# Optimization experiments

Measured on AMD Instinct MI355X. Metric: run time of the kernel, lower is better.

Reference implementation:

```python
import jax, jax.numpy as jnp
import numpy as np


def xnorm(x, g):
    # x * gamma / ||x||_2 along last dim (no eps, matching torch.norm)
    n = jnp.sqrt(jnp.sum(x * x, axis=-1, keepdims=True))
    return x * g / n


def setup_inputs() -> dict:
    key = jax.random.key(0)
    ks = jax.random.split(key, 6)
    B, N, D = 8, 8192, 512
    H, DK, DV = 8, 64, 64
    std = 0.001
    return {
        "queries": jax.random.normal(ks[0], (B, N, D), dtype=jnp.float32),
        # weights stored [in, out] (transposed vs torch Linear)
        "Wq": jax.random.normal(ks[1], (D, H * DK), dtype=jnp.float32) * std,
        "bq": jnp.zeros((H * DK,), dtype=jnp.float32),
        "Wk": jax.random.normal(ks[2], (D, H * DK), dtype=jnp.float32) * std,
        "bk": jnp.zeros((H * DK,), dtype=jnp.float32),
        "Wv": jax.random.normal(ks[3], (D, H * DV), dtype=jnp.float32) * std,
        "bv": jnp.zeros((H * DV,), dtype=jnp.float32),
        "Wo": jax.random.normal(ks[4], (H * DV, D), dtype=jnp.float32) * std,
        "bo": jnp.zeros((D,), dtype=jnp.float32),
        "gamma": jax.random.normal(ks[5], (1, H, 1, 1), dtype=jnp.float32),
    }


def reference(queries, Wq, bq, Wk, bk, Wv, bv, Wo, bo, gamma):
    B, N, D = queries.shape
    H, DK = 8, 64
    DV = 64
    q = (queries @ Wq + bq).reshape(B, N, H, DK)  # bnhd
    k = (queries @ Wk + bk).reshape(B, N, H, DK)
    v = (queries @ Wv + bv).reshape(B, N, H, DV)
    # kv = k^T @ v per (batch, head): [B,H,DK,DV]
    kv = jnp.einsum("bnhk,bnhv->bhkv", k, v)
    kv_n = xnorm(kv, gamma)                       # norm over DV axis
    q_n = xnorm(q.transpose(0, 2, 1, 3), gamma)   # bhnd, norm over DK axis
    out = jnp.einsum("bhnk,bhkv->bnhv", q_n, kv_n).reshape(B, N, H * DV)
    return out @ Wo + bo
```

## Files before the change

### kernel.cpp

```cpp
#include <hip/hip_runtime.h>

typedef __attribute__((ext_vector_type(8))) short s8v;
typedef __attribute__((ext_vector_type(4))) short s4v;
typedef __attribute__((ext_vector_type(4))) float f4v;

__device__ __forceinline__ unsigned short f2bf(float f) {
  unsigned int u = __float_as_uint(f);
  u += 0x7FFFu + ((u >> 16) & 1u);
  return (unsigned short)(u >> 16);
}
__device__ __forceinline__ float bf2f(unsigned short s) {
  return __uint_as_float(((unsigned int)s) << 16);
}

__device__ __forceinline__ void gld16(const void* g, void* l) {
  __builtin_amdgcn_global_load_lds(
      (const __attribute__((address_space(1))) unsigned int*)g,
      (__attribute__((address_space(3))) unsigned int*)l, 16, 0, 0);
}

#define TILE_SYNC() asm volatile("s_waitcnt vmcnt(0) lgkmcnt(0)\n\ts_barrier" ::: "memory")

__global__ __launch_bounds__(256)
void convert_x_kernel(const float* __restrict__ X, unsigned short* __restrict__ Xbf)
{
  size_t base = ((size_t)blockIdx.x * 256 + threadIdx.x) * 8;
  float4 a = *(const float4*)&X[base];
  float4 b = *(const float4*)&X[base + 4];
  s8v p = (s8v){ (short)f2bf(a.x), (short)f2bf(a.y), (short)f2bf(a.z), (short)f2bf(a.w),
                 (short)f2bf(b.x), (short)f2bf(b.y), (short)f2bf(b.z), (short)f2bf(b.w) };
  *(s8v*)&Xbf[base] = p;
}

__global__ __launch_bounds__(256)
void transpose_w_kernel(const float* __restrict__ Wq, const float* __restrict__ Wk,
                        const float* __restrict__ Wv, unsigned short* __restrict__ Wt)
{
  __shared__ float T[64][68];
  const int kt = blockIdx.x, nt = blockIdx.y;
  const float* W = (nt < 8) ? Wq : (nt < 16 ? Wk : Wv);
  const int n0 = (nt & 7) * 64, k0 = kt * 64;
  const int t = threadIdx.x;
  #pragma unroll
  for (int it = 0; it < 4; ++it) {
    int idx = it * 256 + t;
    int k = idx >> 4, n4 = (idx & 15) << 2;
    *(float4*)&T[k][n4] = *(const float4*)&W[(size_t)(k0 + k) * 512 + n0 + n4];
  }
  __syncthreads();
  #pragma unroll
  for (int it = 0; it < 2; ++it) {
    int idx = it * 256 + t;
    int n = idx >> 3, k8 = (idx & 7) << 3;
    s8v p;
    #pragma unroll
    for (int j = 0; j < 8; ++j) p[j] = (short)f2bf(T[k8 + j][n]);
    *(s8v*)&Wt[((size_t)nt * 64 + n) * 512 + k0 + k8] = p;
  }
}

__global__ __launch_bounds__(256, 2)
void gemm_qkv_kernel(const unsigned short* __restrict__ Xbf,
                     const unsigned short* __restrict__ Wt,
                     const float* __restrict__ bq, const float* __restrict__ bk,
                     const float* __restrict__ bv,
                     const float* __restrict__ gamma,
                     unsigned short* __restrict__ qkv)
{
  __shared__ short As[2][8192];
  __shared__ short Bs[2][8192];
  const int t = threadIdx.x;
  const int o = blockIdx.x;
  const int swz = (o & 7) * 768 + (o >> 3);
  const int nb = swz % 12, rb = swz / 12;
  const int wave = t >> 6, lane = t & 63;
  const int wm = wave & 1, wn = wave >> 1;
  const int quad = lane >> 4, l16 = lane & 15;
  const int row0 = rb * 128;
  const int ncol0 = nb * 128;

  const unsigned short* ap[4];
  const unsigned short* bp[4];
  int ldst[4];
  #pragma unroll
  for (int i = 0; i < 4; ++i) {
    int s = i * 256 + t;
    int m = s >> 3;
    int kb = (s & 7) ^ (m & 7);
    ap[i] = Xbf + (size_t)(row0 + m) * 512 + kb * 8;
    bp[i] = Wt + (size_t)(ncol0 + m) * 512 + kb * 8;
    ldst[i] = s * 8;
  }

  f4v acc[4][4];
  #pragma unroll
  for (int i = 0; i < 4; ++i)
    #pragma unroll
    for (int j = 0; j < 4; ++j) acc[i][j] = (f4v){0.f, 0.f, 0.f, 0.f};

  #pragma unroll
  for (int i = 0; i < 4; ++i) {
    gld16(ap[i], &As[0][ldst[i]]);
    gld16(bp[i], &Bs[0][ldst[i]]);
  }
  TILE_SYNC();

  for (int kt = 0; kt < 8; ++kt) {
    const int cur = kt & 1;
    if (kt < 7) {
      const int koff = (kt + 1) * 64;
      #pragma unroll
      for (int i = 0; i < 4; ++i) {
        gld16(ap[i] + koff, &As[cur ^ 1][ldst[i]]);
        gld16(bp[i] + koff, &Bs[cur ^ 1][ldst[i]]);
      }
    }
    #pragma unroll
    for (int ks = 0; ks < 2; ++ks) {
      s8v a[4], b[4];
      #pragma unroll
      for (int mi = 0; mi < 4; ++mi) {
        int r = wm * 64 + mi * 16 + l16;
        int slot = r * 8 + ((ks * 4 + quad) ^ (r & 7));
        a[mi] = *(const s8v*)&As[cur][slot * 8];
      }
      #pragma unroll
      for (int nj = 0; nj < 4; ++nj) {
        int r = wn * 64 + nj * 16 + l16;
        int slot = r * 8 + ((ks * 4 + quad) ^ (r & 7));
        b[nj] = *(const s8v*)&Bs[cur][slot * 8];
      }
      #pragma unroll
      for (int mi = 0; mi < 4; ++mi)
        #pragma unroll
        for (int nj = 0; nj < 4; ++nj)
          acc[mi][nj] = __builtin_amdgcn_mfma_f32_16x16x32_bf16(a[mi], b[nj], acc[mi][nj], 0, 0, 0);
    }
    TILE_SYNC();
  }

  #pragma unroll
  for (int nj = 0; nj < 4; ++nj) {
    int colg = ncol0 + wn * 64 + nj * 16 + l16;
    float bias;
    if (colg < 512) bias = bq[colg];
    else if (colg < 1024) bias = bk[colg - 512];
    else bias = bv[colg - 1024];
    #pragma unroll
    for (int mi = 0; mi < 4; ++mi) {
      acc[mi][nj][0] += bias; acc[mi][nj][1] += bias;
      acc[mi][nj][2] += bias; acc[mi][nj][3] += bias;
    }
  }

  if (nb < 4) {
    float g = gamma[nb * 2 + wn];
    #pragma unroll
    for (int mi = 0; mi < 4; ++mi)
      #pragma unroll
      for (int rr = 0; rr < 4; ++rr) {
        float ss = acc[mi][0][rr] * acc[mi][0][rr] + acc[mi][1][rr] * acc[mi][1][rr]
                 + acc[mi][2][rr] * acc[mi][2][rr] + acc[mi][3][rr] * acc[mi][3][rr];
        ss += __shfl_xor(ss, 1);
        ss += __shfl_xor(ss, 2);
        ss += __shfl_xor(ss, 4);
        ss += __shfl_xor(ss, 8);
        float scale = g * rsqrtf(ss);
        acc[mi][0][rr] *= scale; acc[mi][1][rr] *= scale;
        acc[mi][2][rr] *= scale; acc[mi][3][rr] *= scale;
      }
  }

  const int colbase = ncol0 + wn * 64;
  #pragma unroll
  for (int mi = 0; mi < 4; ++mi)
    #pragma unroll
    for (int nj = 0; nj < 4; ++nj)
      #pragma unroll
      for (int rr = 0; rr < 4; ++rr) {
        int row = row0 + wm * 64 + mi * 16 + quad * 4 + rr;
        int col = colbase + nj * 16 + l16;
        qkv[(size_t)row * 1536 + col] = f2bf(acc[mi][nj][rr]);
      }
}

__global__ __launch_bounds__(256)
void kv_accum_kernel(const unsigned short* __restrict__ qkv, float* __restrict__ kvpart)
{
  __shared__ float ksf[16][64];
  __shared__ float vsf[16][64];
  const int t = threadIdx.x;
  const int bh = blockIdx.x, chunk = blockIdx.y;
  const int b = bh >> 3, h = bh & 7;
  const int base_row = b * 8192 + chunk * 512;
  const int lane = t & 63, wave = t >> 6;
  const int dk0 = (lane & 7) * 8, dv0 = (lane >> 3) * 8;
  const int half = t >> 7, tt = t & 127;
  const int sr = tt >> 3, u = tt & 7;
  const int col = (half ? 1024 : 512) + h * 64 + u * 8;
  const unsigned short* src = qkv + (size_t)(base_row + sr) * 1536 + col;
  float* dstlds = half ? &vsf[sr][u * 8] : &ksf[sr][u * 8];
  float acc[8][8] = {};

  for (int it = 0; it < 32; ++it) {
    __syncthreads();
    union { int4 v; unsigned short s[8]; } raw;
    raw.v = *(const int4*)(src + (size_t)it * 16 * 1536);
    float4 lo = { bf2f(raw.s[0]), bf2f(raw.s[1]), bf2f(raw.s[2]), bf2f(raw.s[3]) };
    float4 hi = { bf2f(raw.s[4]), bf2f(raw.s[5]), bf2f(raw.s[6]), bf2f(raw.s[7]) };
    *(float4*)dstlds = lo;
    *(float4*)(dstlds + 4) = hi;
    __syncthreads();
    #pragma unroll
    for (int rr = 0; rr < 4; ++rr) {
      int r = rr * 4 + wave;
      float4 ka = *(const float4*)&ksf[r][dk0];
      float4 kb = *(const float4*)&ksf[r][dk0 + 4];
      float4 va = *(const float4*)&vsf[r][dv0];
      float4 vb = *(const float4*)&vsf[r][dv0 + 4];
      float kf[8] = { ka.x, ka.y, ka.z, ka.w, kb.x, kb.y, kb.z, kb.w };
      float vf[8] = { va.x, va.y, va.z, va.w, vb.x, vb.y, vb.z, vb.w };
      #pragma unroll
      for (int i = 0; i < 8; ++i)
        #pragma unroll
        for (int j = 0; j < 8; ++j)
          acc[i][j] = fmaf(kf[i], vf[j], acc[i][j]);
    }
  }
  float* dst = kvpart + ((size_t)(chunk * 4 + wave) * 64 + bh) * 4096;
  #pragma unroll
  for (int i = 0; i < 8; ++i) {
    *(float4*)&dst[(dk0 + i) * 64 + dv0]     = (float4){ acc[i][0], acc[i][1], acc[i][2], acc[i][3] };
    *(float4*)&dst[(dk0 + i) * 64 + dv0 + 4] = (float4){ acc[i][4], acc[i][5], acc[i][6], acc[i][7] };
  }
}

__global__ __launch_bounds__(256)
void kv_reduce_kernel(const float* __restrict__ kvpart, float* __restrict__ kvbuf)
{
  const int bh = blockIdx.x, seg = blockIdx.y, t = threadIdx.x;
  #pragma unroll
  for (int e = 0; e < 2; ++e) {
    int i = seg * 512 + e * 256 + t;
    float s = 0.f;
    for (int c = 0; c < 64; ++c) s += kvpart[((size_t)c * 64 + bh) * 4096 + i];
    kvbuf[(size_t)bh * 4096 + i] = s;
  }
}

__global__ __launch_bounds__(256)
void build_w2t_kernel(const float* __restrict__ kvbuf, const float* __restrict__ Wo,
                      const float* __restrict__ gamma, unsigned short* __restrict__ W2t)
{
  __shared__ float WoS[512][16];
  const int b = blockIdx.x, dt = blockIdx.y;
  const int d0 = dt * 16;
  const int t = threadIdx.x;
  for (int i = 0; i < 32; ++i) {
    int flat = i * 256 + t;
    int rr_ = flat >> 4, c = flat & 15;
    WoS[rr_][c] = Wo[(size_t)rr_ * 512 + d0 + c];
  }
  __syncthreads();
  for (int rr = 0; rr < 2; ++rr) {
    int r = rr * 256 + t;
    int h = r >> 6, k = r & 63;
    const float* krow = kvbuf + ((size_t)b * 8 + h) * 4096 + (size_t)k * 64;
    float ss = 0.f;
    #pragma unroll
    for (int v = 0; v < 64; v += 4) {
      float4 x = *(const float4*)&krow[v];
      ss += x.x * x.x + x.y * x.y + x.z * x.z + x.w * x.w;
    }
    float scale = gamma[h] * rsqrtf(ss);
    f4v accv[4];
    #pragma unroll
    for (int j = 0; j < 4; ++j) accv[j] = (f4v){0.f, 0.f, 0.f, 0.f};
    for (int v = 0; v < 64; ++v) {
      float m = krow[v] * scale;
      const float* w = &WoS[h * 64 + v][0];
      #pragma unroll
      for (int j4 = 0; j4 < 4; ++j4) {
        float4 ww = *(const float4*)&w[j4 * 4];
        accv[j4][0] = fmaf(m, ww.x, accv[j4][0]);
        accv[j4][1] = fmaf(m, ww.y, accv[j4][1]);
        accv[j4][2] = fmaf(m, ww.z, accv[j4][2]);
        accv[j4][3] = fmaf(m, ww.w, accv[j4][3]);
      }
    }
    #pragma unroll
    for (int j = 0; j < 16; ++j)
      W2t[((size_t)b * 512 + d0 + j) * 512 + r] = f2bf(accv[j >> 2][j & 3]);
  }
}

__global__ __launch_bounds__(256, 2)
void gemm_out_kernel(const unsigned short* __restrict__ qkv,
                     const unsigned short* __restrict__ W2t,
                     const float* __restrict__ bo,
                     float* __restrict__ out)
{
  __shared__ short As[2][8192];
  __shared__ short Bs[2][8192];
  const int t = threadIdx.x;
  const int o = blockIdx.x;
  const int swz = (o & 7) * 256 + (o >> 3);
  const int nb = swz & 3, rb = swz >> 2;
  const int wave = t >> 6, lane = t & 63;
  const int wm = wave & 1, wn = wave >> 1;
  const int quad = lane >> 4, l16 = lane & 15;
  const int row0 = rb * 128;
  const int ncol0 = nb * 128;
  const unsigned short* Wb = W2t + (size_t)(rb >> 6) * 262144;

  const unsigned short* ap[4];
  const unsigned short* bp[4];
  int ldst[4];
  #pragma unroll
  for (int i = 0; i < 4; ++i) {
    int s = i * 256 + t;
    int m = s >> 3;
    int kb = (s & 7) ^ (m & 7);
    ap[i] = qkv + (size_t)(row0 + m) * 1536 + kb * 8;
    bp[i] = Wb + (size_t)(ncol0 + m) * 512 + kb * 8;
    ldst[i] = s * 8;
  }

  f4v acc[4][4];
  #pragma unroll
  for (int i = 0; i < 4; ++i)
    #pragma unroll
    for (int j = 0; j < 4; ++j) acc[i][j] = (f4v){0.f, 0.f, 0.f, 0.f};

  #pragma unroll
  for (int i = 0; i < 4; ++i) {
    gld16(ap[i], &As[0][ldst[i]]);
    gld16(bp[i], &Bs[0][ldst[i]]);
  }
  TILE_SYNC();

  for (int kt = 0; kt < 8; ++kt) {
    const int cur = kt & 1;
    if (kt < 7) {
      const int koff = (kt + 1) * 64;
      #pragma unroll
      for (int i = 0; i < 4; ++i) {
        gld16(ap[i] + koff, &As[cur ^ 1][ldst[i]]);
        gld16(bp[i] + koff, &Bs[cur ^ 1][ldst[i]]);
      }
    }
    #pragma unroll
    for (int ks = 0; ks < 2; ++ks) {
      s8v a[4], b[4];
      #pragma unroll
      for (int mi = 0; mi < 4; ++mi) {
        int r = wm * 64 + mi * 16 + l16;
        int slot = r * 8 + ((ks * 4 + quad) ^ (r & 7));
        a[mi] = *(const s8v*)&As[cur][slot * 8];
      }
      #pragma unroll
      for (int nj = 0; nj < 4; ++nj) {
        int r = wn * 64 + nj * 16 + l16;
        int slot = r * 8 + ((ks * 4 + quad) ^ (r & 7));
        b[nj] = *(const s8v*)&Bs[cur][slot * 8];
      }
      #pragma unroll
      for (int mi = 0; mi < 4; ++mi)
        #pragma unroll
        for (int nj = 0; nj < 4; ++nj)
          acc[mi][nj] = __builtin_amdgcn_mfma_f32_16x16x32_bf16(a[mi], b[nj], acc[mi][nj], 0, 0, 0);
    }
    TILE_SYNC();
  }

  const int colbase = ncol0 + wn * 64;
  #pragma unroll
  for (int nj = 0; nj < 4; ++nj) {
    float bias = bo[colbase + nj * 16 + l16];
    #pragma unroll
    for (int mi = 0; mi < 4; ++mi)
      #pragma unroll
      for (int rr = 0; rr < 4; ++rr) {
        int row = row0 + wm * 64 + mi * 16 + quad * 4 + rr;
        int col = colbase + nj * 16 + l16;
        out[(size_t)row * 512 + col] = acc[mi][nj][rr] + bias;
      }
  }
}

extern "C" void kernel_launch(void* const* d_in, const int* in_sizes, int n_in,
                              void* d_out, int out_size, void* d_ws, size_t ws_size,
                              hipStream_t stream)
{
  (void)in_sizes; (void)n_in; (void)out_size; (void)ws_size;
  const float* X     = (const float*)d_in[0];
  const float* Wq    = (const float*)d_in[1];
  const float* bq    = (const float*)d_in[2];
  const float* Wk    = (const float*)d_in[3];
  const float* bk    = (const float*)d_in[4];
  const float* Wv    = (const float*)d_in[5];
  const float* bv    = (const float*)d_in[6];
  const float* Wo    = (const float*)d_in[7];
  const float* bo    = (const float*)d_in[8];
  const float* gamma = (const float*)d_in[9];

  char* ws = (char*)d_ws;
  unsigned short* qkv = (unsigned short*)ws;
  unsigned short* Xbf = (unsigned short*)(ws + 201326592);
  float* kvpart = (float*)(ws + 201326592);
  unsigned short* Wt  = (unsigned short*)(ws + 201326592 + 67108864);
  float* kvbuf        = (float*)(ws + 201326592 + 67108864 + 1572864);
  unsigned short* W2t = (unsigned short*)(ws + 201326592 + 67108864 + 1572864 + 1048576);

  dim3 blk(256);
  convert_x_kernel<<<16384, blk, 0, stream>>>(X, Xbf);
  transpose_w_kernel<<<dim3(8, 24), blk, 0, stream>>>(Wq, Wk, Wv, Wt);
  gemm_qkv_kernel<<<6144, blk, 0, stream>>>(Xbf, Wt, bq, bk, bv, gamma, qkv);
  kv_accum_kernel<<<dim3(64, 16), blk, 0, stream>>>(qkv, kvpart);
  kv_reduce_kernel<<<dim3(64, 8), blk, 0, stream>>>(kvpart, kvbuf);
  build_w2t_kernel<<<dim3(8, 32), blk, 0, stream>>>(kvbuf, Wo, gamma, W2t);
  gemm_out_kernel<<<2048, blk, 0, stream>>>(qkv, W2t, bo, (float*)d_out);
}
```

Baseline: 551.9 us.

## Enlarge GEMM tiles to 256x256 with 8 waves and interleaved prefetch

Both bf16 GEMMs move from 128x128 tiles with 4 waves to 256x256 tiles with 8 waves (512 threads), so each wave computes a 128x64 output block. This raises operand reuse per LDS byte and cuts the block count by four. The K-loop is split into four MFMA phases with the next-tile global-to-LDS loads spread across them, barriers between phases, and s_setprio raised around the MFMA bursts. The cost is higher register pressure (8x4 accumulators), 128KB of LDS per block, which limits occupancy, and fewer blocks for load balancing.

```diff
diff --git a/kernel.cpp b/kernel.cpp
--- a/kernel.cpp
+++ b/kernel.cpp
@@ -59,7 +59,7 @@
   }
 }
 
-__global__ __launch_bounds__(256, 2)
+__global__ __launch_bounds__(512, 2)
 void gemm_qkv_kernel(const unsigned short* __restrict__ Xbf,
                      const unsigned short* __restrict__ Wt,
                      const float* __restrict__ bq, const float* __restrict__ bk,
@@ -67,34 +67,32 @@
                      const float* __restrict__ gamma,
                      unsigned short* __restrict__ qkv)
 {
-  __shared__ short As[2][8192];
-  __shared__ short Bs[2][8192];
+  __shared__ short As[2][16384];
+  __shared__ short Bs[2][16384];
   const int t = threadIdx.x;
   const int o = blockIdx.x;
-  const int swz = (o & 7) * 768 + (o >> 3);
-  const int nb = swz % 12, rb = swz / 12;
+  const int swz = (o & 7) * 192 + (o >> 3);
+  const int nb = swz % 6, rb = swz / 6;
   const int wave = t >> 6, lane = t & 63;
   const int wm = wave & 1, wn = wave >> 1;
   const int quad = lane >> 4, l16 = lane & 15;
-  const int row0 = rb * 128;
-  const int ncol0 = nb * 128;
+  const int row0 = rb * 256, ncol0 = nb * 256;
 
   const unsigned short* ap[4];
   const unsigned short* bp[4];
   int ldst[4];
   #pragma unroll
   for (int i = 0; i < 4; ++i) {
-    int s = i * 256 + t;
-    int m = s >> 3;
-    int kb = (s & 7) ^ (m & 7);
+    int s = i * 512 + t;
+    int m = s >> 3, kb = (s & 7) ^ (m & 7);
     ap[i] = Xbf + (size_t)(row0 + m) * 512 + kb * 8;
     bp[i] = Wt + (size_t)(ncol0 + m) * 512 + kb * 8;
     ldst[i] = s * 8;
   }
 
-  f4v acc[4][4];
-  #pragma unroll
-  for (int i = 0; i < 4; ++i)
+  f4v acc[8][4];
+  #pragma unroll
+  for (int i = 0; i < 8; ++i)
     #pragma unroll
     for (int j = 0; j < 4; ++j) acc[i][j] = (f4v){0.f, 0.f, 0.f, 0.f};
 
@@ -107,35 +105,89 @@
 
   for (int kt = 0; kt < 8; ++kt) {
     const int cur = kt & 1;
-    if (kt < 7) {
-      const int koff = (kt + 1) * 64;
-      #pragma unroll
-      for (int i = 0; i < 4; ++i) {
-        gld16(ap[i] + koff, &As[cur ^ 1][ldst[i]]);
-        gld16(bp[i] + koff, &Bs[cur ^ 1][ldst[i]]);
-      }
-    }
-    #pragma unroll
-    for (int ks = 0; ks < 2; ++ks) {
-      s8v a[4], b[4];
-      #pragma unroll
-      for (int mi = 0; mi < 4; ++mi) {
-        int r = wm * 64 + mi * 16 + l16;
-        int slot = r * 8 + ((ks * 4 + quad) ^ (r & 7));
-        a[mi] = *(const s8v*)&As[cur][slot * 8];
-      }
-      #pragma unroll
-      for (int nj = 0; nj < 4; ++nj) {
+    const short* Ac = As[cur];
+    const short* Bc = Bs[cur];
+    short* An = (short*)As[cur ^ 1];
+    short* Bn = (short*)Bs[cur ^ 1];
+    const int koff = (kt + 1) * 64;
+    const bool pf = kt < 7;
+    s8v afr[4][2], bfr[4][2];
+
+    if (pf) {
+      gld16(ap[0] + koff, &An[ldst[0]]);
+      gld16(ap[1] + koff, &An[ldst[1]]);
+      gld16(bp[0] + koff, &Bn[ldst[0]]);
+      gld16(bp[1] + koff, &Bn[ldst[1]]);
+    }
+    #pragma unroll
+    for (int nj = 0; nj < 4; ++nj)
+      #pragma unroll
+      for (int ks = 0; ks < 2; ++ks) {
         int r = wn * 64 + nj * 16 + l16;
-        int slot = r * 8 + ((ks * 4 + quad) ^ (r & 7));
-        b[nj] = *(const s8v*)&Bs[cur][slot * 8];
-      }
-      #pragma unroll
-      for (int mi = 0; mi < 4; ++mi)
-        #pragma unroll
-        for (int nj = 0; nj < 4; ++nj)
-          acc[mi][nj] = __builtin_amdgcn_mfma_f32_16x16x32_bf16(a[mi], b[nj], acc[mi][nj], 0, 0, 0);
-    }
+        bfr[nj][ks] = *(const s8v*)&Bc[(r * 8 + ((ks * 4 + quad) ^ (r & 7))) * 8];
+      }
+    #pragma unroll
+    for (int mi = 0; mi < 4; ++mi)
+      #pragma unroll
+      for (int ks = 0; ks < 2; ++ks) {
+        int r = wm * 128 + mi * 16 + l16;
+        afr[mi][ks] = *(const s8v*)&Ac[(r * 8 + ((ks * 4 + quad) ^ (r & 7))) * 8];
+      }
+    __builtin_amdgcn_s_setprio(1);
+    #pragma unroll
+    for (int mi = 0; mi < 4; ++mi)
+      #pragma unroll
+      for (int nj = 0; nj < 2; ++nj)
+        #pragma unroll
+        for (int ks = 0; ks < 2; ++ks)
+          acc[mi][nj] = __builtin_amdgcn_mfma_f32_16x16x32_bf16(afr[mi][ks], bfr[nj][ks], acc[mi][nj], 0, 0, 0);
+    __builtin_amdgcn_s_setprio(0);
+    __builtin_amdgcn_s_barrier();
+
+    if (pf) {
+      gld16(ap[2] + koff, &An[ldst[2]]);
+      gld16(ap[3] + koff, &An[ldst[3]]);
+      gld16(bp[2] + koff, &Bn[ldst[2]]);
+      gld16(bp[3] + koff, &Bn[ldst[3]]);
+    }
+    __builtin_amdgcn_s_setprio(1);
+    #pragma unroll
+    for (int mi = 0; mi < 4; ++mi)
+      #pragma unroll
+      for (int nj = 2; nj < 4; ++nj)
+        #pragma unroll
+        for (int ks = 0; ks < 2; ++ks)
+          acc[mi][nj] = __builtin_amdgcn_mfma_f32_16x16x32_bf16(afr[mi][ks], bfr[nj][ks], acc[mi][nj], 0, 0, 0);
+    __builtin_amdgcn_s_setprio(0);
+    __builtin_amdgcn_s_barrier();
+
+    #pragma unroll
+    for (int mi = 0; mi < 4; ++mi)
+      #pragma unroll
+      for (int ks = 0; ks < 2; ++ks) {
+        int r = wm * 128 + (4 + mi) * 16 + l16;
+        afr[mi][ks] = *(const s8v*)&Ac[(r * 8 + ((ks * 4 + quad) ^ (r & 7))) * 8];
+      }
+    __builtin_amdgcn_s_setprio(1);
+    #pragma unroll
+    for (int mi = 0; mi < 4; ++mi)
+      #pragma unroll
+      for (int nj = 0; nj < 2; ++nj)
+        #pragma unroll
+        for (int ks = 0; ks < 2; ++ks)
+          acc[4 + mi][nj] = __builtin_amdgcn_mfma_f32_16x16x32_bf16(afr[mi][ks], bfr[nj][ks], acc[4 + mi][nj], 0, 0, 0);
+    __builtin_amdgcn_s_setprio(0);
+    __builtin_amdgcn_s_barrier();
+
+    __builtin_amdgcn_s_setprio(1);
+    #pragma unroll
+    for (int mi = 0; mi < 4; ++mi)
+      #pragma unroll
+      for (int nj = 2; nj < 4; ++nj)
+        #pragma unroll
+        for (int ks = 0; ks < 2; ++ks)
+          acc[4 + mi][nj] = __builtin_amdgcn_mfma_f32_16x16x32_bf16(afr[mi][ks], bfr[nj][ks], acc[4 + mi][nj], 0, 0, 0);
+    __builtin_amdgcn_s_setprio(0);
     TILE_SYNC();
   }
 
@@ -147,16 +199,16 @@
     else if (colg < 1024) bias = bk[colg - 512];
     else bias = bv[colg - 1024];
     #pragma unroll
-    for (int mi = 0; mi < 4; ++mi) {
+    for (int mi = 0; mi < 8; ++mi) {
       acc[mi][nj][0] += bias; acc[mi][nj][1] += bias;
       acc[mi][nj][2] += bias; acc[mi][nj][3] += bias;
     }
   }
 
-  if (nb < 4) {
-    float g = gamma[nb * 2 + wn];
-    #pragma unroll
-    for (int mi = 0; mi < 4; ++mi)
+  if (nb < 2) {
+    float g = gamma[nb * 4 + wn];
+    #pragma unroll
+    for (int mi = 0; mi < 8; ++mi)
       #pragma unroll
       for (int rr = 0; rr < 4; ++rr) {
         float ss = acc[mi][0][rr] * acc[mi][0][rr] + acc[mi][1][rr] * acc[mi][1][rr]
@@ -173,12 +225,12 @@
 
   const int colbase = ncol0 + wn * 64;
   #pragma unroll
-  for (int mi = 0; mi < 4; ++mi)
+  for (int mi = 0; mi < 8; ++mi)
     #pragma unroll
     for (int nj = 0; nj < 4; ++nj)
       #pragma unroll
       for (int rr = 0; rr < 4; ++rr) {
-        int row = row0 + wm * 64 + mi * 16 + quad * 4 + rr;
+        int row = row0 + wm * 128 + mi * 16 + quad * 4 + rr;
         int col = colbase + nj * 16 + l16;
         qkv[(size_t)row * 1536 + col] = f2bf(acc[mi][nj][rr]);
       }
@@ -294,41 +346,39 @@
   }
 }
 
-__global__ __launch_bounds__(256, 2)
+__global__ __launch_bounds__(512, 2)
 void gemm_out_kernel(const unsigned short* __restrict__ qkv,
                      const unsigned short* __restrict__ W2t,
                      const float* __restrict__ bo,
                      float* __restrict__ out)
 {
-  __shared__ short As[2][8192];
-  __shared__ short Bs[2][8192];
+  __shared__ short As[2][16384];
+  __shared__ short Bs[2][16384];
   const int t = threadIdx.x;
   const int o = blockIdx.x;
-  const int swz = (o & 7) * 256 + (o >> 3);
-  const int nb = swz & 3, rb = swz >> 2;
+  const int swz = (o & 7) * 64 + (o >> 3);
+  const int nb = swz & 1, rb = swz >> 1;
   const int wave = t >> 6, lane = t & 63;
   const int wm = wave & 1, wn = wave >> 1;
   const int quad = lane >> 4, l16 = lane & 15;
-  const int row0 = rb * 128;
-  const int ncol0 = nb * 128;
-  const unsigned short* Wb = W2t + (size_t)(rb >> 6) * 262144;
+  const int row0 = rb * 256, ncol0 = nb * 256;
+  const unsigned short* Wb = W2t + (size_t)(rb >> 5) * 262144;
 
   const unsigned short* ap[4];
   const unsigned short* bp[4];
   int ldst[4];
   #pragma unroll
   for (int i = 0; i < 4; ++i) {
-    int s = i * 256 + t;
-    int m = s >> 3;
-    int kb = (s & 7) ^ (m & 7);
+    int s = i * 512 + t;
+    int m = s >> 3, kb = (s & 7) ^ (m & 7);
     ap[i] = qkv + (size_t)(row0 + m) * 1536 + kb * 8;
     bp[i] = Wb + (size_t)(ncol0 + m) * 512 + kb * 8;
     ldst[i] = s * 8;
   }
 
-  f4v acc[4][4];
-  #pragma unroll
-  for (int i = 0; i < 4; ++i)
+  f4v acc[8][4];
+  #pragma unroll
+  for (int i = 0; i < 8; ++i)
     #pragma unroll
     for (int j = 0; j < 4; ++j) acc[i][j] = (f4v){0.f, 0.f, 0.f, 0.f};
 
@@ -341,35 +391,89 @@
 
   for (int kt = 0; kt < 8; ++kt) {
     const int cur = kt & 1;
-    if (kt < 7) {
-      const int koff = (kt + 1) * 64;
-      #pragma unroll
-      for (int i = 0; i < 4; ++i) {
-        gld16(ap[i] + koff, &As[cur ^ 1][ldst[i]]);
-        gld16(bp[i] + koff, &Bs[cur ^ 1][ldst[i]]);
-      }
-    }
-    #pragma unroll
-    for (int ks = 0; ks < 2; ++ks) {
-      s8v a[4], b[4];
-      #pragma unroll
-      for (int mi = 0; mi < 4; ++mi) {
-        int r = wm * 64 + mi * 16 + l16;
-        int slot = r * 8 + ((ks * 4 + quad) ^ (r & 7));
-        a[mi] = *(const s8v*)&As[cur][slot * 8];
-      }
-      #pragma unroll
-      for (int nj = 0; nj < 4; ++nj) {
+    const short* Ac = As[cur];
+    const short* Bc = Bs[cur];
+    short* An = (short*)As[cur ^ 1];
+    short* Bn = (short*)Bs[cur ^ 1];
+    const int koff = (kt + 1) * 64;
+    const bool pf = kt < 7;
+    s8v afr[4][2], bfr[4][2];
+
+    if (pf) {
+      gld16(ap[0] + koff, &An[ldst[0]]);
+      gld16(ap[1] + koff, &An[ldst[1]]);
+      gld16(bp[0] + koff, &Bn[ldst[0]]);
+      gld16(bp[1] + koff, &Bn[ldst[1]]);
+    }
+    #pragma unroll
+    for (int nj = 0; nj < 4; ++nj)
+      #pragma unroll
+      for (int ks = 0; ks < 2; ++ks) {
         int r = wn * 64 + nj * 16 + l16;
-        int slot = r * 8 + ((ks * 4 + quad) ^ (r & 7));
-        b[nj] = *(const s8v*)&Bs[cur][slot * 8];
-      }
-      #pragma unroll
-      for (int mi = 0; mi < 4; ++mi)
-        #pragma unroll
-        for (int nj = 0; nj < 4; ++nj)
-          acc[mi][nj] = __builtin_amdgcn_mfma_f32_16x16x32_bf16(a[mi], b[nj], acc[mi][nj], 0, 0, 0);
-    }
+        bfr[nj][ks] = *(const s8v*)&Bc[(r * 8 + ((ks * 4 + quad) ^ (r & 7))) * 8];
+      }
+    #pragma unroll
+    for (int mi = 0; mi < 4; ++mi)
+      #pragma unroll
+      for (int ks = 0; ks < 2; ++ks) {
+        int r = wm * 128 + mi * 16 + l16;
+        afr[mi][ks] = *(const s8v*)&Ac[(r * 8 + ((ks * 4 + quad) ^ (r & 7))) * 8];
+      }
+    __builtin_amdgcn_s_setprio(1);
+    #pragma unroll
+    for (int mi = 0; mi < 4; ++mi)
+      #pragma unroll
+      for (int nj = 0; nj < 2; ++nj)
+        #pragma unroll
+        for (int ks = 0; ks < 2; ++ks)
+          acc[mi][nj] = __builtin_amdgcn_mfma_f32_16x16x32_bf16(afr[mi][ks], bfr[nj][ks], acc[mi][nj], 0, 0, 0);
+    __builtin_amdgcn_s_setprio(0);
+    __builtin_amdgcn_s_barrier();
+
+    if (pf) {
+      gld16(ap[2] + koff, &An[ldst[2]]);
+      gld16(ap[3] + koff, &An[ldst[3]]);
+      gld16(bp[2] + koff, &Bn[ldst[2]]);
+      gld16(bp[3] + koff, &Bn[ldst[3]]);
+    }
+    __builtin_amdgcn_s_setprio(1);
+    #pragma unroll
+    for (int mi = 0; mi < 4; ++mi)
+      #pragma unroll
+      for (int nj = 2; nj < 4; ++nj)
+        #pragma unroll
+        for (int ks = 0; ks < 2; ++ks)
+          acc[mi][nj] = __builtin_amdgcn_mfma_f32_16x16x32_bf16(afr[mi][ks], bfr[nj][ks], acc[mi][nj], 0, 0, 0);
+    __builtin_amdgcn_s_setprio(0);
+    __builtin_amdgcn_s_barrier();
+
+    #pragma unroll
+    for (int mi = 0; mi < 4; ++mi)
+      #pragma unroll
+      for (int ks = 0; ks < 2; ++ks) {
+        int r = wm * 128 + (4 + mi) * 16 + l16;
+        afr[mi][ks] = *(const s8v*)&Ac[(r * 8 + ((ks * 4 + quad) ^ (r & 7))) * 8];
+      }
+    __builtin_amdgcn_s_setprio(1);
+    #pragma unroll
+    for (int mi = 0; mi < 4; ++mi)
+      #pragma unroll
+      for (int nj = 0; nj < 2; ++nj)
+        #pragma unroll
+        for (int ks = 0; ks < 2; ++ks)
+          acc[4 + mi][nj] = __builtin_amdgcn_mfma_f32_16x16x32_bf16(afr[mi][ks], bfr[nj][ks], acc[4 + mi][nj], 0, 0, 0);
+    __builtin_amdgcn_s_setprio(0);
+    __builtin_amdgcn_s_barrier();
+
+    __builtin_amdgcn_s_setprio(1);
+    #pragma unroll
+    for (int mi = 0; mi < 4; ++mi)
+      #pragma unroll
+      for (int nj = 2; nj < 4; ++nj)
+        #pragma unroll
+        for (int ks = 0; ks < 2; ++ks)
+          acc[4 + mi][nj] = __builtin_amdgcn_mfma_f32_16x16x32_bf16(afr[mi][ks], bfr[nj][ks], acc[4 + mi][nj], 0, 0, 0);
+    __builtin_amdgcn_s_setprio(0);
     TILE_SYNC();
   }
 
@@ -378,10 +482,10 @@
   for (int nj = 0; nj < 4; ++nj) {
     float bias = bo[colbase + nj * 16 + l16];
     #pragma unroll
-    for (int mi = 0; mi < 4; ++mi)
+    for (int mi = 0; mi < 8; ++mi)
       #pragma unroll
       for (int rr = 0; rr < 4; ++rr) {
-        int row = row0 + wm * 64 + mi * 16 + quad * 4 + rr;
+        int row = row0 + wm * 128 + mi * 16 + quad * 4 + rr;
         int col = colbase + nj * 16 + l16;
         out[(size_t)row * 512 + col] = acc[mi][nj][rr] + bias;
       }
@@ -415,9 +519,9 @@
   dim3 blk(256);
   convert_x_kernel<<<16384, blk, 0, stream>>>(X, Xbf);
   transpose_w_kernel<<<dim3(8, 24), blk, 0, stream>>>(Wq, Wk, Wv, Wt);
-  gemm_qkv_kernel<<<6144, blk, 0, stream>>>(Xbf, Wt, bq, bk, bv, gamma, qkv);
+  gemm_qkv_kernel<<<1536, dim3(512), 0, stream>>>(Xbf, Wt, bq, bk, bv, gamma, qkv);
   kv_accum_kernel<<<dim3(64, 16), blk, 0, stream>>>(qkv, kvpart);
   kv_reduce_kernel<<<dim3(64, 8), blk, 0, stream>>>(kvpart, kvbuf);
   build_w2t_kernel<<<dim3(8, 32), blk, 0, stream>>>(kvbuf, Wo, gamma, W2t);
-  gemm_out_kernel<<<2048, blk, 0, stream>>>(qkv, W2t, bo, (float*)d_out);
-}
+  gemm_out_kernel<<<512, dim3(512), 0, stream>>>(qkv, W2t, bo, (float*)d_out);
+}
```

Result: faster. 530.6 us (-3.8%).
